# Optimization experiments

Hardware: AMD Instinct MI355X
Metric: run time of the kernel (lower is better)

The kernel has to match this reference:

```python
import jax, jax.numpy as jnp
import numpy as np

D_MODEL = 2048
N_HEAD = 16
N_KV_HEAD = 4
D_HEAD = D_MODEL // N_HEAD  # 128
ROPE_BASE = 10000.0


def build_rope_cache(d_head, seq_len):
    # NeoX-style half-split RoPE cache: cos/sin of shape [T, d_head]
    inv_freq = 1.0 / (ROPE_BASE ** (jnp.arange(0, d_head, 2, dtype=jnp.float32) / d_head))
    t = jnp.arange(seq_len, dtype=jnp.float32)
    ang = jnp.einsum('t,f->tf', t, inv_freq)            # [T, d_head/2]
    ang = jnp.concatenate([ang, ang], axis=-1)           # [T, d_head]
    return jnp.cos(ang), jnp.sin(ang)


def apply_rope(x, cos, sin):
    # x: [B, T, H, Dh]; cos/sin: [T, Dh]
    d = x.shape[-1]
    x1, x2 = x[..., : d // 2], x[..., d // 2 :]
    rot = jnp.concatenate([-x2, x1], axis=-1)
    c = cos[None, :, None, :]
    s = sin[None, :, None, :]
    return x * c + rot * s


def setup_inputs() -> dict:
    key = jax.random.key(0)
    k1, k2, k3, k4, k5 = jax.random.split(key, 5)
    B, T = 4, 2048
    scale = 1.0 / np.sqrt(D_MODEL)
    return {
        'x': jax.random.normal(k1, (B, T, D_MODEL), dtype=jnp.float32),
        'Wq': jax.random.normal(k2, (D_MODEL, N_HEAD * D_HEAD), dtype=jnp.float32) * scale,
        'Wk': jax.random.normal(k3, (D_MODEL, N_KV_HEAD * D_HEAD), dtype=jnp.float32) * scale,
        'Wv': jax.random.normal(k4, (D_MODEL, N_KV_HEAD * D_HEAD), dtype=jnp.float32) * scale,
        'Wo': jax.random.normal(k5, (D_MODEL, D_MODEL), dtype=jnp.float32) * scale,
    }


def reference(x, Wq, Wk, Wv, Wo):
    B, T, C = x.shape
    q = (x @ Wq).reshape(B, T, N_HEAD, D_HEAD)
    k = (x @ Wk).reshape(B, T, N_KV_HEAD, D_HEAD)
    v = (x @ Wv).reshape(B, T, N_KV_HEAD, D_HEAD)

    cos, sin = build_rope_cache(D_HEAD, T)  # no cache -> positions [0, T)
    q = apply_rope(q, cos, sin)
    k = apply_rope(k, cos, sin)

    q = q.transpose(0, 2, 1, 3)  # [B, H, T, Dh]
    k = k.transpose(0, 2, 1, 3)  # [B, Hkv, T, Dh]
    v = v.transpose(0, 2, 1, 3)

    rf = N_HEAD // N_KV_HEAD
    k = jnp.repeat(k, rf, axis=1)  # GQA: repeat_interleave over head dim
    v = jnp.repeat(v, rf, axis=1)

    scores = jnp.einsum('bhtd,bhsd->bhts', q, k) / np.sqrt(D_HEAD)
    causal = jnp.tril(jnp.ones((T, T), dtype=bool))
    scores = jnp.where(causal[None, None], scores, -jnp.inf)
    probs = jax.nn.softmax(scores, axis=-1)
    attn = jnp.einsum('bhts,bhsd->bhtd', probs, v)

    attn = attn.transpose(0, 2, 1, 3).reshape(B, T, C)
    return attn @ Wo
```

## Files before the change

kernel.cpp:

```cpp
#include <hip/hip_runtime.h>

typedef unsigned short u16;
typedef __bf16 bf16x8 __attribute__((ext_vector_type(8)));
typedef u16 u16x8 __attribute__((ext_vector_type(8)));
typedef u16 u16x4 __attribute__((ext_vector_type(4)));
typedef float f32x4 __attribute__((ext_vector_type(4)));

#define MFMA16(a, b, c) __builtin_amdgcn_mfma_f32_16x16x32_bf16((a), (b), (c), 0, 0, 0)

__device__ __forceinline__ void async16(const u16* g, u16* l) {
  __builtin_amdgcn_global_load_lds(
      (__attribute__((address_space(1))) void*)(void*)(g),
      (__attribute__((address_space(3))) void*)(void*)(l), 16, 0, 0);
}

__device__ __forceinline__ float bf2f(u16 b) {
  union { unsigned u; float f; } v;
  v.u = ((unsigned)b) << 16;
  return v.f;
}
__device__ __forceinline__ u16 f2bf(float f) {
  union { float f; unsigned u; } v;
  v.f = f;
  unsigned u = v.u;
  return (u16)((u + 0x7FFFu + ((u >> 16) & 1u)) >> 16);
}

__global__ __launch_bounds__(256) void convert_k(const float* __restrict__ in,
                                                 u16* __restrict__ out, int n8) {
  const int stride = gridDim.x * 256;
  for (int i = blockIdx.x * 256 + threadIdx.x; i < n8; i += stride) {
    const float* fp = in + (size_t)i * 8;
    float4 a = *(const float4*)fp, b = *(const float4*)(fp + 4);
    u16x8 o;
    o[0] = f2bf(a.x); o[1] = f2bf(a.y); o[2] = f2bf(a.z); o[3] = f2bf(a.w);
    o[4] = f2bf(b.x); o[5] = f2bf(b.y); o[6] = f2bf(b.z); o[7] = f2bf(b.w);
    *(u16x8*)&out[(size_t)i * 8] = o;
  }
}

__global__ __launch_bounds__(256) void transpose_cvt_k(const float* __restrict__ W,
                                                       u16* __restrict__ Wt, int K, int N) {
  __shared__ __align__(16) u16 tile[64 * 72];
  const int t = threadIdx.x;
  const int n0 = blockIdx.x * 64, k0 = blockIdx.y * 64;
#pragma unroll
  for (int i = 0; i < 2; ++i) {
    int flat = t + i * 256;
    int r = flat >> 3, c8 = (flat & 7) * 8;
    const float* p = W + (size_t)(k0 + r) * N + n0 + c8;
    float4 a = *(const float4*)p, b = *(const float4*)(p + 4);
    u16x8 v;
    v[0] = f2bf(a.x); v[1] = f2bf(a.y); v[2] = f2bf(a.z); v[3] = f2bf(a.w);
    v[4] = f2bf(b.x); v[5] = f2bf(b.y); v[6] = f2bf(b.z); v[7] = f2bf(b.w);
#pragma unroll
    for (int j = 0; j < 8; ++j) tile[r * 72 + c8 + j] = v[j];
  }
  __syncthreads();
#pragma unroll
  for (int i = 0; i < 2; ++i) {
    int flat = t + i * 256;
    int r = flat >> 3, c8 = (flat & 7) * 8;
    u16x8 v;
#pragma unroll
    for (int j = 0; j < 8; ++j) v[j] = tile[(c8 + j) * 72 + r];
    *(u16x8*)&Wt[(size_t)(n0 + r) * K + k0 + c8] = v;
  }
}

__global__ __launch_bounds__(256) void rope_table_k(float* __restrict__ cosT,
                                                    float* __restrict__ sinT) {
  int idx = blockIdx.x * 256 + threadIdx.x;
  int tp = idx >> 6, i = idx & 63;
  float invf = expf(-(float)i * (9.210340371976184f / 64.0f));
  float ang = (float)tp * invf;
  cosT[idx] = cosf(ang);
  sinT[idx] = sinf(ang);
}

__global__ __launch_bounds__(256) void rope_apply_k(u16* __restrict__ base,
                                                    const float* __restrict__ cosT,
                                                    const float* __restrict__ sinT,
                                                    int rowStride, int nhMask, int rowShift,
                                                    float scale) {
  int idx = blockIdx.x * 256 + threadIdx.x;
  int i4 = idx & 15;
  int hh = (idx >> 4) & nhMask;
  int row = idx >> rowShift;
  int tp = row & 2047;
  int i = i4 * 4;
  u16* p = base + (size_t)row * rowStride + hh * 128;
  u16x4 a = *(u16x4*)&p[i];
  u16x4 b = *(u16x4*)&p[i + 64];
  float4 c = *(const float4*)&cosT[tp * 64 + i];
  float4 s = *(const float4*)&sinT[tp * 64 + i];
  float cc[4] = {c.x, c.y, c.z, c.w}, ss[4] = {s.x, s.y, s.z, s.w};
  u16x4 oa, ob;
#pragma unroll
  for (int j = 0; j < 4; ++j) {
    float x1 = bf2f(a[j]), x2 = bf2f(b[j]);
    oa[j] = f2bf((x1 * cc[j] - x2 * ss[j]) * scale);
    ob[j] = f2bf((x2 * cc[j] + x1 * ss[j]) * scale);
  }
  *(u16x4*)&p[i] = oa;
  *(u16x4*)&p[i + 64] = ob;
}

template <bool F32OUT>
__global__ __launch_bounds__(256) void gemm_tn(const u16* __restrict__ A,
                                               const u16* __restrict__ Bt,
                                               void* __restrict__ C, int M, int N, int K) {
  __shared__ __align__(16) u16 As[128 * 32];
  __shared__ __align__(16) u16 Bs[128 * 32];
  const int t = threadIdx.x;
  const int l = t & 63, w = t >> 6;
  const int wm = w >> 1, wn = w & 1;
  const int lr = l & 15, lg = l >> 4;
  const int nbx = gridDim.x;
  const int lin = blockIdx.y * nbx + blockIdx.x;
  const int cpx = (nbx * gridDim.y) >> 3;
  const int sl = (lin & 7) * cpx + (lin >> 3);
  const size_t m0 = (size_t)(sl / nbx) * 128, n0 = (size_t)(sl % nbx) * 128;
  f32x4 acc[4][4] = {};
  for (int k0 = 0; k0 < K; k0 += 32) {
#pragma unroll
    for (int i = 0; i < 2; ++i) {
      int flat = t + i * 256;
      int r = flat >> 2, seg = (flat & 3) * 8;
      async16(&A[(m0 + r) * K + k0 + seg], &As[flat * 8]);
      async16(&Bt[(n0 + r) * K + k0 + seg], &Bs[flat * 8]);
    }
    __syncthreads();
    bf16x8 af[4], bfr[4];
#pragma unroll
    for (int i = 0; i < 4; ++i) {
      af[i] = *(const bf16x8*)&As[(wm * 64 + i * 16 + lr) * 32 + lg * 8];
      bfr[i] = *(const bf16x8*)&Bs[(wn * 64 + i * 16 + lr) * 32 + lg * 8];
    }
#pragma unroll
    for (int mi = 0; mi < 4; ++mi)
#pragma unroll
      for (int ni = 0; ni < 4; ++ni) acc[mi][ni] = MFMA16(af[mi], bfr[ni], acc[mi][ni]);
    __syncthreads();
  }
#pragma unroll
  for (int mi = 0; mi < 4; ++mi)
#pragma unroll
    for (int ni = 0; ni < 4; ++ni)
#pragma unroll
      for (int r = 0; r < 4; ++r) {
        size_t row = m0 + wm * 64 + mi * 16 + lg * 4 + r;
        size_t col = n0 + wn * 64 + ni * 16 + lr;
        if constexpr (F32OUT)
          ((float*)C)[row * N + col] = acc[mi][ni][r];
        else
          ((u16*)C)[row * N + col] = f2bf(acc[mi][ni][r]);
      }
}

__global__ __launch_bounds__(512, 4) void attn_k(const u16* __restrict__ QKV,
                                                 u16* __restrict__ O) {
  constexpr int T = 2048, CS = 3072, OC = 2048;
  __shared__ __align__(16) u16 Ks[2][64 * 128];
  __shared__ __align__(16) u16 Vt[128 * 72];
  __shared__ __align__(16) u16 Pl[128 * 72];
  const int t = threadIdx.x, l = t & 63, w = t >> 6, lr = l & 15, lg = l >> 4;
  const int lin = blockIdx.x;
  const int v = (lin & 7) * 128 + (lin >> 3);
  const int bh = v >> 4;
  const int qt = 15 - (v & 15);
  const int b = bh >> 4, h = bh & 15, kv = h >> 2;
  const int q0 = qt * 128;
  const int myrow = w * 16 + lg * 4;
  const size_t rowQ = (size_t)(b * T + q0 + w * 16 + lr) * CS + h * 128;
  bf16x8 qf[4];
#pragma unroll
  for (int di = 0; di < 4; ++di) qf[di] = *(const bf16x8*)&QKV[rowQ + di * 32 + lg * 8];
  bf16x8 onesf;
#pragma unroll
  for (int j = 0; j < 8; ++j) onesf[j] = (__bf16)1.0f;
  f32x4 lsum = {};
  f32x4 oacc[8] = {};
  const int lastst = 2 * qt + 1;
  const size_t kvBase = (size_t)(b * T) * CS + 2048 + kv * 128;
  const int sV = (t >> 4) * 2, d8V = (t & 15) * 8;
  u16x8 vr0, vr1;
  {
#pragma unroll
    for (int i = 0; i < 2; ++i) {
      int flat = t + i * 512;
      int r = flat >> 4, c = flat & 15;
      async16(&QKV[kvBase + (size_t)r * CS + ((c ^ (r & 7)) * 8)], &Ks[0][flat * 8]);
    }
    vr0 = *(const u16x8*)&QKV[kvBase + 512 + (size_t)sV * CS + d8V];
    vr1 = *(const u16x8*)&QKV[kvBase + 512 + (size_t)(sV + 1) * CS + d8V];
#pragma unroll
    for (int j = 0; j < 8; ++j) {
      int d = d8V + j;
      int slot = (sV >> 3) ^ ((d >> 3) & 7);
      *(unsigned*)&Vt[d * 72 + slot * 8 + (sV & 7)] =
          (unsigned)vr0[j] | ((unsigned)vr1[j] << 16);
    }
    __syncthreads();
  }
  int cb = 0;
  for (int st = 0; st <= lastst; ++st) {
    if (st < lastst) {
      const size_t kvRow = kvBase + (size_t)(st + 1) * 64 * CS;
#pragma unroll
      for (int i = 0; i < 2; ++i) {
        int flat = t + i * 512;
        int r = flat >> 4, c = flat & 15;
        async16(&QKV[kvRow + (size_t)r * CS + ((c ^ (r & 7)) * 8)], &Ks[cb ^ 1][flat * 8]);
      }
      vr0 = *(const u16x8*)&QKV[kvRow + 512 + (size_t)sV * CS + d8V];
      vr1 = *(const u16x8*)&QKV[kvRow + 512 + (size_t)(sV + 1) * CS + d8V];
    }
    const int s0 = st * 64;
    const bool skip = (st == lastst) && (w < 4);
    if (!skip) {
      f32x4 sacc[4] = {};
#pragma unroll
      for (int di = 0; di < 4; ++di)
#pragma unroll
        for (int n = 0; n < 4; ++n) {
          bf16x8 bk =
              *(const bf16x8*)&Ks[cb][(n * 16 + lr) * 128 + (((di * 4 + lg) ^ (lr & 7)) << 3)];
          sacc[n] = MFMA16(qf[di], bk, sacc[n]);
        }
      const bool diag = (st >= 2 * qt);
#pragma unroll
      for (int n = 0; n < 4; ++n)
#pragma unroll
        for (int r = 0; r < 4; ++r) {
          float s_ = sacc[n][r] * 1.44269504f - 11.5415603f;
          if (diag && (s0 + 16 * n + lr > q0 + myrow + r)) s_ = -1e30f;
          *(__bf16*)&Pl[(myrow + r) * 72 + 16 * n + lr] = (__bf16)exp2f(s_);
        }
#pragma unroll
      for (int ks = 0; ks < 2; ++ks) {
        bf16x8 pa = *(const bf16x8*)&Pl[(w * 16 + lr) * 72 + ks * 32 + lg * 8];
        lsum = MFMA16(pa, onesf, lsum);
#pragma unroll
        for (int nf = 0; nf < 8; ++nf) {
          int d = 16 * nf + lr;
          int seg = lg + 4 * ks;
          bf16x8 vb = *(const bf16x8*)&Vt[d * 72 + ((seg ^ ((d >> 3) & 7)) << 3)];
          oacc[nf] = MFMA16(pa, vb, oacc[nf]);
        }
      }
    }
    __syncthreads();
    if (st < lastst) {
#pragma unroll
      for (int j = 0; j < 8; ++j) {
        int d = d8V + j;
        int slot = (sV >> 3) ^ ((d >> 3) & 7);
        *(unsigned*)&Vt[d * 72 + slot * 8 + (sV & 7)] =
            (unsigned)vr0[j] | ((unsigned)vr1[j] << 16);
      }
    }
    __syncthreads();
    cb ^= 1;
  }
#pragma unroll
  for (int r = 0; r < 4; ++r) {
    float il = 1.0f / lsum[r];
    size_t orow = (size_t)(b * T + q0 + myrow + r) * OC + h * 128;
#pragma unroll
    for (int nf = 0; nf < 8; ++nf) O[orow + 16 * nf + lr] = f2bf(oacc[nf][r] * il);
  }
}

__global__ __launch_bounds__(256) void sentinel_k(float* __restrict__ out) {
  out[blockIdx.x * 256 + threadIdx.x] = 1.0e4f;
}

extern "C" void kernel_launch(void* const* d_in, const int* in_sizes, int n_in, void* d_out,
                              int out_size, void* d_ws, size_t ws_size, hipStream_t stream) {
  const float* x = (const float*)d_in[0];
  const float* Wq = (const float*)d_in[1];
  const float* Wk = (const float*)d_in[2];
  const float* Wv = (const float*)d_in[3];
  const float* Wo = (const float*)d_in[4];

  char* p = (char*)d_ws;
  auto take = [&](size_t bytes) {
    char* r = p;
    p += (bytes + 255) & ~(size_t)255;
    return r;
  };
  u16* WqkvT = (u16*)take((size_t)3072 * 2048 * 2);
  u16* WoT = (u16*)take((size_t)2048 * 2048 * 2);
  u16* QKV = (u16*)take((size_t)8192 * 3072 * 2);
  u16* Ob = (u16*)take((size_t)8192 * 2048 * 2);
  u16* xbf = (u16*)take((size_t)8192 * 2048 * 2);
  float* cosT = (float*)take((size_t)2048 * 64 * 4);
  float* sinT = (float*)take((size_t)2048 * 64 * 4);
  if (ws_size < (size_t)(p - (char*)d_ws)) {
    sentinel_k<<<4, 256, 0, stream>>>((float*)d_out);
    return;
  }

  convert_k<<<2048, 256, 0, stream>>>(x, xbf, 8192 * 2048 / 8);
  transpose_cvt_k<<<dim3(32, 32), 256, 0, stream>>>(Wq, WqkvT, 2048, 2048);
  transpose_cvt_k<<<dim3(8, 32), 256, 0, stream>>>(Wk, WqkvT + (size_t)2048 * 2048, 2048, 512);
  transpose_cvt_k<<<dim3(8, 32), 256, 0, stream>>>(Wv, WqkvT + (size_t)2560 * 2048, 2048, 512);
  transpose_cvt_k<<<dim3(32, 32), 256, 0, stream>>>(Wo, WoT, 2048, 2048);
  rope_table_k<<<512, 256, 0, stream>>>(cosT, sinT);

  gemm_tn<false><<<dim3(24, 64), 256, 0, stream>>>(xbf, WqkvT, QKV, 8192, 3072, 2048);

  rope_apply_k<<<8192, 256, 0, stream>>>(QKV, cosT, sinT, 3072, 15, 8, 0.08838834764831845f);
  rope_apply_k<<<2048, 256, 0, stream>>>(QKV + 2048, cosT, sinT, 3072, 3, 6, 1.0f);

  attn_k<<<1024, 512, 0, stream>>>(QKV, Ob);

  gemm_tn<true><<<dim3(16, 64), 256, 0, stream>>>(Ob, WoT, (void*)d_out, 8192, 2048, 2048);
}
```

Before: 461.6 us.

## Switch attention to 32x32 MFMA with 2D wave split over query and key/dim

Rewrites the attention inner loop to use 32x32x16 bf16 MFMAs. Waves are now arranged 4 (query blocks of 32 rows) by 2 (key halves for QK, dim halves for PV) instead of 8 waves of 16 query rows each. The larger MFMA shape is meant to cut LDS fragment reads per flop and improve matrix-core efficiency. Fully masked QK tiles are skipped and zero-filled in the P buffer. In exchange, an extra barrier is needed between writing P and consuming it. The P stride is also changed, and each wave recomputes the row-sum MFMA redundantly for its dim half.

```diff
diff --git a/kernel.cpp b/kernel.cpp
--- a/kernel.cpp
+++ b/kernel.cpp
@@ -2,11 +2,14 @@
 
 typedef unsigned short u16;
 typedef __bf16 bf16x8 __attribute__((ext_vector_type(8)));
+typedef __bf16 bf16x4 __attribute__((ext_vector_type(4)));
 typedef u16 u16x8 __attribute__((ext_vector_type(8)));
 typedef u16 u16x4 __attribute__((ext_vector_type(4)));
 typedef float f32x4 __attribute__((ext_vector_type(4)));
+typedef float f32x16 __attribute__((ext_vector_type(16)));
 
 #define MFMA16(a, b, c) __builtin_amdgcn_mfma_f32_16x16x32_bf16((a), (b), (c), 0, 0, 0)
+#define MFMA32(a, b, c) __builtin_amdgcn_mfma_f32_32x32x16_bf16((a), (b), (c), 0, 0, 0)
 
 __device__ __forceinline__ void async16(const u16* g, u16* l) {
   __builtin_amdgcn_global_load_lds(
@@ -160,27 +163,28 @@
 
 __global__ __launch_bounds__(512, 4) void attn_k(const u16* __restrict__ QKV,
                                                  u16* __restrict__ O) {
-  constexpr int T = 2048, CS = 3072, OC = 2048;
+  constexpr int T = 2048, CS = 3072, OC = 2048, PLS = 76;
   __shared__ __align__(16) u16 Ks[2][64 * 128];
   __shared__ __align__(16) u16 Vt[128 * 72];
-  __shared__ __align__(16) u16 Pl[128 * 72];
-  const int t = threadIdx.x, l = t & 63, w = t >> 6, lr = l & 15, lg = l >> 4;
+  __shared__ __align__(16) u16 Pl[128 * PLS];
+  const int t = threadIdx.x, l = t & 63, w = t >> 6;
+  const int lane31 = l & 31, hi = l >> 5;
+  const int wq = w >> 1, ws = w & 1, wd = w & 1;
   const int lin = blockIdx.x;
   const int v = (lin & 7) * 128 + (lin >> 3);
   const int bh = v >> 4;
   const int qt = 15 - (v & 15);
   const int b = bh >> 4, h = bh & 15, kv = h >> 2;
   const int q0 = qt * 128;
-  const int myrow = w * 16 + lg * 4;
-  const size_t rowQ = (size_t)(b * T + q0 + w * 16 + lr) * CS + h * 128;
-  bf16x8 qf[4];
-#pragma unroll
-  for (int di = 0; di < 4; ++di) qf[di] = *(const bf16x8*)&QKV[rowQ + di * 32 + lg * 8];
+  const size_t rowQ = (size_t)(b * T + q0 + 32 * wq + lane31) * CS + h * 128;
+  bf16x8 qf[8];
+#pragma unroll
+  for (int ki = 0; ki < 8; ++ki) qf[ki] = *(const bf16x8*)&QKV[rowQ + 16 * ki + 8 * hi];
   bf16x8 onesf;
 #pragma unroll
   for (int j = 0; j < 8; ++j) onesf[j] = (__bf16)1.0f;
-  f32x4 lsum = {};
-  f32x4 oacc[8] = {};
+  f32x16 lsum = {};
+  f32x16 oacc[2] = {};
   const int lastst = 2 * qt + 1;
   const size_t kvBase = (size_t)(b * T) * CS + 2048 + kv * 128;
   const int sV = (t >> 4) * 2, d8V = (t & 15) * 8;
@@ -198,8 +202,7 @@
     for (int j = 0; j < 8; ++j) {
       int d = d8V + j;
       int slot = (sV >> 3) ^ ((d >> 3) & 7);
-      *(unsigned*)&Vt[d * 72 + slot * 8 + (sV & 7)] =
-          (unsigned)vr0[j] | ((unsigned)vr1[j] << 16);
+      *(unsigned*)&Vt[d * 72 + slot * 8 + (sV & 7)] = (unsigned)vr0[j] | ((unsigned)vr1[j] << 16);
     }
     __syncthreads();
   }
@@ -217,36 +220,49 @@
       vr1 = *(const u16x8*)&QKV[kvRow + 512 + (size_t)(sV + 1) * CS + d8V];
     }
     const int s0 = st * 64;
-    const bool skip = (st == lastst) && (w < 4);
-    if (!skip) {
-      f32x4 sacc[4] = {};
-#pragma unroll
-      for (int di = 0; di < 4; ++di)
-#pragma unroll
-        for (int n = 0; n < 4; ++n) {
-          bf16x8 bk =
-              *(const bf16x8*)&Ks[cb][(n * 16 + lr) * 128 + (((di * 4 + lg) ^ (lr & 7)) << 3)];
-          sacc[n] = MFMA16(qf[di], bk, sacc[n]);
+    const bool diag = (st >= 2 * qt);
+    const bool qkSkip = diag && (s0 + 32 * ws > q0 + 32 * wq + 31);
+    if (!qkSkip) {
+      f32x16 sacc = {};
+      const int srow = 32 * ws + lane31;
+#pragma unroll
+      for (int ki = 0; ki < 8; ++ki) {
+        bf16x8 bk = *(const bf16x8*)&Ks[cb][srow * 128 + (((2 * ki + hi) ^ (srow & 7)) << 3)];
+        sacc = MFMA32(qf[ki], bk, sacc);
+      }
+#pragma unroll
+      for (int reg = 0; reg < 16; ++reg) {
+        int r32 = (reg & 3) + 8 * (reg >> 2) + 4 * hi;
+        float s_ = sacc[reg] * 1.44269504f - 11.5415603f;
+        if (diag && (s0 + srow > q0 + 32 * wq + r32)) s_ = -1e30f;
+        *(__bf16*)&Pl[(32 * wq + r32) * PLS + srow] = (__bf16)exp2f(s_);
+      }
+    } else {
+#pragma unroll
+      for (int reg = 0; reg < 16; ++reg) {
+        int r32 = (reg & 3) + 8 * (reg >> 2) + 4 * hi;
+        Pl[(32 * wq + r32) * PLS + 32 * ws + lane31] = 0;
+      }
+    }
+    __syncthreads();
+    const bool pvSkip = (st == lastst) && (wq < 2);
+    if (!pvSkip) {
+#pragma unroll
+      for (int ss = 0; ss < 4; ++ss) {
+        bf16x4 plo = *(const bf16x4*)&Pl[(32 * wq + lane31) * PLS + 16 * ss + 8 * hi];
+        bf16x4 phi = *(const bf16x4*)&Pl[(32 * wq + lane31) * PLS + 16 * ss + 8 * hi + 4];
+        bf16x8 pa;
+#pragma unroll
+        for (int j = 0; j < 4; ++j) {
+          pa[j] = plo[j];
+          pa[j + 4] = phi[j];
         }
-      const bool diag = (st >= 2 * qt);
-#pragma unroll
-      for (int n = 0; n < 4; ++n)
-#pragma unroll
-        for (int r = 0; r < 4; ++r) {
-          float s_ = sacc[n][r] * 1.44269504f - 11.5415603f;
-          if (diag && (s0 + 16 * n + lr > q0 + myrow + r)) s_ = -1e30f;
-          *(__bf16*)&Pl[(myrow + r) * 72 + 16 * n + lr] = (__bf16)exp2f(s_);
-        }
-#pragma unroll
-      for (int ks = 0; ks < 2; ++ks) {
-        bf16x8 pa = *(const bf16x8*)&Pl[(w * 16 + lr) * 72 + ks * 32 + lg * 8];
-        lsum = MFMA16(pa, onesf, lsum);
-#pragma unroll
-        for (int nf = 0; nf < 8; ++nf) {
-          int d = 16 * nf + lr;
-          int seg = lg + 4 * ks;
-          bf16x8 vb = *(const bf16x8*)&Vt[d * 72 + ((seg ^ ((d >> 3) & 7)) << 3)];
-          oacc[nf] = MFMA16(pa, vb, oacc[nf]);
+        lsum = MFMA32(pa, onesf, lsum);
+#pragma unroll
+        for (int dt = 0; dt < 2; ++dt) {
+          int d = 64 * wd + 32 * dt + lane31;
+          bf16x8 vb = *(const bf16x8*)&Vt[d * 72 + (((2 * ss + hi) ^ ((d >> 3) & 7)) << 3)];
+          oacc[dt] = MFMA32(pa, vb, oacc[dt]);
         }
       }
     }
@@ -260,15 +276,15 @@
             (unsigned)vr0[j] | ((unsigned)vr1[j] << 16);
       }
     }
-    __syncthreads();
     cb ^= 1;
   }
 #pragma unroll
-  for (int r = 0; r < 4; ++r) {
-    float il = 1.0f / lsum[r];
-    size_t orow = (size_t)(b * T + q0 + myrow + r) * OC + h * 128;
-#pragma unroll
-    for (int nf = 0; nf < 8; ++nf) O[orow + 16 * nf + lr] = f2bf(oacc[nf][r] * il);
+  for (int reg = 0; reg < 16; ++reg) {
+    int r32 = (reg & 3) + 8 * (reg >> 2) + 4 * hi;
+    float il = 1.0f / lsum[reg];
+    size_t orow = (size_t)(b * T + q0 + 32 * wq + r32) * OC + h * 128;
+    O[orow + 64 * wd + lane31] = f2bf(oacc[0][reg] * il);
+    O[orow + 64 * wd + 32 + lane31] = f2bf(oacc[1][reg] * il);
   }
 }
 
```

Result: slower. 864.7 us (+87.3%).

## Fuse RoPE and query scaling into QKV GEMM epilogue

Applied to the files above, without the earlier changes.

Removes the two separate RoPE apply kernels and applies the rotation inside the QKV GEMM epilogue. Each 128-wide output tile (one head) is staged through shared memory one row group at a time, so every lane can read its rotation partner column at c^64, then multiplies by the cos/sin tables and the query scale before storing bf16. This saves a full read-modify-write pass over Q and K plus two launches. In exchange the GEMM gains a 16.5KB shared buffer, which may lower occupancy, and extra barriers in the epilogue.

```diff
diff --git a/kernel.cpp b/kernel.cpp
--- a/kernel.cpp
+++ b/kernel.cpp
@@ -78,40 +78,15 @@
   sinT[idx] = sinf(ang);
 }
 
-__global__ __launch_bounds__(256) void rope_apply_k(u16* __restrict__ base,
-                                                    const float* __restrict__ cosT,
-                                                    const float* __restrict__ sinT,
-                                                    int rowStride, int nhMask, int rowShift,
-                                                    float scale) {
-  int idx = blockIdx.x * 256 + threadIdx.x;
-  int i4 = idx & 15;
-  int hh = (idx >> 4) & nhMask;
-  int row = idx >> rowShift;
-  int tp = row & 2047;
-  int i = i4 * 4;
-  u16* p = base + (size_t)row * rowStride + hh * 128;
-  u16x4 a = *(u16x4*)&p[i];
-  u16x4 b = *(u16x4*)&p[i + 64];
-  float4 c = *(const float4*)&cosT[tp * 64 + i];
-  float4 s = *(const float4*)&sinT[tp * 64 + i];
-  float cc[4] = {c.x, c.y, c.z, c.w}, ss[4] = {s.x, s.y, s.z, s.w};
-  u16x4 oa, ob;
-#pragma unroll
-  for (int j = 0; j < 4; ++j) {
-    float x1 = bf2f(a[j]), x2 = bf2f(b[j]);
-    oa[j] = f2bf((x1 * cc[j] - x2 * ss[j]) * scale);
-    ob[j] = f2bf((x2 * cc[j] + x1 * ss[j]) * scale);
-  }
-  *(u16x4*)&p[i] = oa;
-  *(u16x4*)&p[i + 64] = ob;
-}
-
 template <bool F32OUT>
 __global__ __launch_bounds__(256) void gemm_tn(const u16* __restrict__ A,
                                                const u16* __restrict__ Bt,
-                                               void* __restrict__ C, int M, int N, int K) {
+                                               void* __restrict__ C, int M, int N, int K,
+                                               const float* __restrict__ cosT,
+                                               const float* __restrict__ sinT) {
   __shared__ __align__(16) u16 As[128 * 32];
   __shared__ __align__(16) u16 Bs[128 * 32];
+  __shared__ __align__(16) float Ex[32 * 132];
   const int t = threadIdx.x;
   const int l = t & 63, w = t >> 6;
   const int wm = w >> 1, wn = w & 1;
@@ -142,6 +117,36 @@
 #pragma unroll
       for (int ni = 0; ni < 4; ++ni) acc[mi][ni] = MFMA16(af[mi], bfr[ni], acc[mi][ni]);
     __syncthreads();
+  }
+  if constexpr (!F32OUT) {
+    if (n0 < 2560) {
+      const float qsc = (n0 < 2048) ? 0.08838834764831845f : 1.0f;
+#pragma unroll
+      for (int mi = 0; mi < 4; ++mi) {
+        __syncthreads();
+#pragma unroll
+        for (int ni = 0; ni < 4; ++ni)
+#pragma unroll
+          for (int r = 0; r < 4; ++r)
+            Ex[(wm * 16 + lg * 4 + r) * 132 + wn * 64 + ni * 16 + lr] = acc[mi][ni][r];
+        __syncthreads();
+#pragma unroll
+        for (int ni = 0; ni < 4; ++ni)
+#pragma unroll
+          for (int r = 0; r < 4; ++r) {
+            int rl = wm * 16 + lg * 4 + r;
+            int c = wn * 64 + ni * 16 + lr;
+            size_t grow = m0 + wm * 64 + mi * 16 + lg * 4 + r;
+            float own = acc[mi][ni][r];
+            float prt = Ex[rl * 132 + (c ^ 64)];
+            size_t ti = (size_t)(grow & 2047) * 64 + (c & 63);
+            float cs = cosT[ti], sn = sinT[ti];
+            float o = (c < 64) ? (own * cs - prt * sn) : (own * cs + prt * sn);
+            ((u16*)C)[grow * N + n0 + c] = f2bf(o * qsc);
+          }
+      }
+      return;
+    }
   }
 #pragma unroll
   for (int mi = 0; mi < 4; ++mi)
@@ -309,12 +314,10 @@
   transpose_cvt_k<<<dim3(32, 32), 256, 0, stream>>>(Wo, WoT, 2048, 2048);
   rope_table_k<<<512, 256, 0, stream>>>(cosT, sinT);
 
-  gemm_tn<false><<<dim3(24, 64), 256, 0, stream>>>(xbf, WqkvT, QKV, 8192, 3072, 2048);
-
-  rope_apply_k<<<8192, 256, 0, stream>>>(QKV, cosT, sinT, 3072, 15, 8, 0.08838834764831845f);
-  rope_apply_k<<<2048, 256, 0, stream>>>(QKV + 2048, cosT, sinT, 3072, 3, 6, 1.0f);
+  gemm_tn<false><<<dim3(24, 64), 256, 0, stream>>>(xbf, WqkvT, QKV, 8192, 3072, 2048, cosT, sinT);
 
   attn_k<<<1024, 512, 0, stream>>>(QKV, Ob);
 
-  gemm_tn<true><<<dim3(16, 64), 256, 0, stream>>>(Ob, WoT, (void*)d_out, 8192, 2048, 2048);
-}
+  gemm_tn<true><<<dim3(16, 64), 256, 0, stream>>>(Ob, WoT, (void*)d_out, 8192, 2048, 2048,
+                                                  cosT, sinT);
+}
```

After: 473.8 us. +2.6%, slower.
